# Kernel optimization log

Measured on AMD Instinct MI355X. Metric: run time of the kernel, lower is better.

The kernel has to match this reference:

```python
import jax, jax.numpy as jnp
import numpy as np

N_NODES = 50000
N_EDGES = 640000
F = 128          # feat_dims == hidden_dims == out_channels
L = 5            # num_layers of GatedGraphConv


def setup_inputs() -> dict:
    key = jax.random.key(0)
    ks = jax.random.split(key, 9)
    s = 1.0 / np.sqrt(F)
    x = jax.random.normal(ks[0], (N_NODES, F), dtype=jnp.float32)
    edge_index = jax.random.randint(ks[1], (2, N_EDGES), 0, N_NODES, dtype=jnp.int64)
    weight = jax.random.uniform(ks[2], (L, F, F), jnp.float32, -s, s)   # per-layer linear
    w_ih = jax.random.uniform(ks[3], (3 * F, F), jnp.float32, -s, s)     # GRUCell input weights
    w_hh = jax.random.uniform(ks[4], (3 * F, F), jnp.float32, -s, s)     # GRUCell hidden weights
    b_ih = jax.random.uniform(ks[5], (3 * F,), jnp.float32, -s, s)
    b_hh = jax.random.uniform(ks[6], (3 * F,), jnp.float32, -s, s)
    lin_w = jax.random.uniform(ks[7], (1, F), jnp.float32, -s, s)
    lin_b = jax.random.uniform(ks[8], (1,), jnp.float32, -s, s)
    return {"x": x, "edge_index": edge_index, "weight": weight,
            "w_ih": w_ih, "w_hh": w_hh, "b_ih": b_ih, "b_hh": b_hh,
            "lin_w": lin_w, "lin_b": lin_b}


def _gru_cell(m, h, w_ih, w_hh, b_ih, b_hh):
    gi = m @ w_ih.T + b_ih          # [N, 3F]
    gh = h @ w_hh.T + b_hh          # [N, 3F]
    i_r, i_z, i_n = jnp.split(gi, 3, axis=-1)
    h_r, h_z, h_n = jnp.split(gh, 3, axis=-1)
    r = jax.nn.sigmoid(i_r + h_r)
    z = jax.nn.sigmoid(i_z + h_z)
    n = jnp.tanh(i_n + r * h_n)
    return (1.0 - z) * n + z * h


def reference(x, edge_index, weight, w_ih, w_hh, b_ih, b_hh, lin_w, lin_b):
    src = edge_index[0]   # message source (x_j)
    dst = edge_index[1]   # aggregation target
    n_nodes = x.shape[0]
    h = x  # in_channels == out_channels, no padding needed
    for i in range(L):
        m = h @ weight[i]                                   # [N, F]
        agg = jax.ops.segment_sum(m[src], dst, num_segments=n_nodes)  # add-aggregate
        h = _gru_cell(agg, h, w_ih, w_hh, b_ih, b_hh)
    out = jax.nn.relu(h) @ lin_w.T + lin_b                  # [N, 1]
    return out
```

## Files before the change

### kernel.cpp

```cpp
#include <hip/hip_runtime.h>

typedef float f32x4 __attribute__((ext_vector_type(4)));
typedef __bf16 bf16x8 __attribute__((ext_vector_type(8)));
typedef unsigned short u16x8 __attribute__((ext_vector_type(8)));

#define F 128

__device__ __forceinline__ unsigned short bf16_rne(float f) {
  unsigned u = __float_as_uint(f);
  u += 0x7FFFu + ((u >> 16) & 1u);
  return (unsigned short)(u >> 16);
}
__device__ __forceinline__ float bf16f(unsigned short s) {
  return __uint_as_float((unsigned)s << 16);
}

__global__ void split8_kernel(const float* __restrict__ in,
                              unsigned short* __restrict__ hi, unsigned short* __restrict__ lo,
                              int n8) {
  int i = blockIdx.x * 256 + threadIdx.x;
  if (i >= n8) return;
  const float4* p = (const float4*)in + 2 * (size_t)i;
  float4 a = p[0], b = p[1];
  float v[8] = {a.x, a.y, a.z, a.w, b.x, b.y, b.z, b.w};
  u16x8 vh, vl;
#pragma unroll
  for (int e = 0; e < 8; ++e) {
    unsigned short x = bf16_rne(v[e]);
    vh[e] = x;
    vl[e] = bf16_rne(v[e] - bf16f(x));
  }
  *(u16x8*)(hi + 8 * (size_t)i) = vh;
  *(u16x8*)(lo + 8 * (size_t)i) = vl;
}

__device__ __forceinline__ int pidx(int j, int k) {
  int ks = k >> 5;
  int lane = (j & 15) | (((k >> 3) & 3) << 4);
  return (ks * 24 + (j >> 4)) * 512 + lane * 8 + (k & 7);
}

__global__ void prep_w_kernel(const float* __restrict__ W, const float* __restrict__ w_ih,
                              const float* __restrict__ w_hh,
                              unsigned short* __restrict__ WcT_hi, unsigned short* __restrict__ WcT_lo,
                              unsigned short* __restrict__ Whh_hi, unsigned short* __restrict__ Whh_lo,
                              int L) {
  int idx = blockIdx.x * 256 + threadIdx.x;
  const int per_layer = 384 * 128;
  if (idx < L * per_layer) {
    int t = idx / per_layer;
    int r = idx - t * per_layer;
    int j = r >> 7;
    int k = r & 127;
    const float* wi = w_ih + (size_t)j * 128;
    const float* wk = W + (size_t)t * 16384 + (size_t)k * 128;
    float acc = 0.f;
#pragma unroll 4
    for (int c = 0; c < 128; ++c) acc = fmaf(wk[c], wi[c], acc);
    unsigned short x = bf16_rne(acc);
    int p = t * per_layer + pidx(j, k);
    WcT_hi[p] = x;
    WcT_lo[p] = bf16_rne(acc - bf16f(x));
  } else if (idx < L * per_layer + per_layer) {
    int r = idx - L * per_layer;
    int j = r >> 7, k = r & 127;
    float v = w_hh[r];
    unsigned short x = bf16_rne(v);
    int p = pidx(j, k);
    Whh_hi[p] = x;
    Whh_lo[p] = bf16_rne(v - bf16f(x));
  }
}

__global__ void hist_kernel(const int* __restrict__ ei, int* __restrict__ cnt, int E) {
  int e = blockIdx.x * 256 + threadIdx.x;
  if (e < E) atomicAdd(&cnt[ei[E + e]], 1);
}

__global__ void scan1_kernel(const int* __restrict__ cnt, int* __restrict__ exscan,
                             int* __restrict__ chunk_sums, int N) {
  __shared__ int tmp[256];
  int i = blockIdx.x * 256 + threadIdx.x;
  int v = (i < N) ? cnt[i] : 0;
  tmp[threadIdx.x] = v;
  __syncthreads();
#pragma unroll
  for (int off = 1; off < 256; off <<= 1) {
    int a = (threadIdx.x >= off) ? tmp[threadIdx.x - off] : 0;
    __syncthreads();
    tmp[threadIdx.x] += a;
    __syncthreads();
  }
  if (i < N) exscan[i] = tmp[threadIdx.x] - v;
  if (threadIdx.x == 255) chunk_sums[blockIdx.x] = tmp[255];
}

__global__ void scan2_kernel(int* __restrict__ chunk_sums, int nchunk) {
  __shared__ int tmp[256];
  int v = (threadIdx.x < nchunk) ? chunk_sums[threadIdx.x] : 0;
  tmp[threadIdx.x] = v;
  __syncthreads();
#pragma unroll
  for (int off = 1; off < 256; off <<= 1) {
    int a = (threadIdx.x >= off) ? tmp[threadIdx.x - off] : 0;
    __syncthreads();
    tmp[threadIdx.x] += a;
    __syncthreads();
  }
  if (threadIdx.x < nchunk) chunk_sums[threadIdx.x] = tmp[threadIdx.x] - v;
}

__global__ void finalize_rowptr_kernel(const int* __restrict__ exscan,
                                       const int* __restrict__ chunk_sums,
                                       int* __restrict__ rowptr, int* __restrict__ cursor,
                                       int N, int E) {
  int i = blockIdx.x * 256 + threadIdx.x;
  if (i < N) {
    int v = exscan[i] + chunk_sums[i >> 8];
    rowptr[i] = v;
    cursor[i] = v;
  }
  if (i == N) rowptr[N] = E;
}

__global__ void place_kernel(const int* __restrict__ ei, int* __restrict__ cursor,
                             int* __restrict__ csr_src, int E) {
  int e = blockIdx.x * 256 + threadIdx.x;
  if (e >= E) return;
  int pos = atomicAdd(&cursor[ei[E + e]], 1);
  csr_src[pos] = ei[e];
}

__global__ __launch_bounds__(256) void gather_kernel(
    const unsigned* __restrict__ hh, const unsigned* __restrict__ hl,
    const int* __restrict__ rowptr, const int* __restrict__ csr_src,
    unsigned* __restrict__ shi, unsigned* __restrict__ slo, int N) {
  int node = blockIdx.x * 4 + (threadIdx.x >> 6);
  if (node >= N) return;
  int d = threadIdx.x & 63;
  int beg = rowptr[node], end = rowptr[node + 1];
  float a0 = 0.f, a1 = 0.f;
  int j = beg;
  for (; j + 4 <= end; j += 4) {
    int s0 = csr_src[j], s1 = csr_src[j + 1], s2 = csr_src[j + 2], s3 = csr_src[j + 3];
    unsigned h0 = hh[(size_t)s0 * 64 + d], l0 = hl[(size_t)s0 * 64 + d];
    unsigned h1 = hh[(size_t)s1 * 64 + d], l1 = hl[(size_t)s1 * 64 + d];
    unsigned h2 = hh[(size_t)s2 * 64 + d], l2 = hl[(size_t)s2 * 64 + d];
    unsigned h3 = hh[(size_t)s3 * 64 + d], l3 = hl[(size_t)s3 * 64 + d];
    a0 += bf16f(h0 & 0xffff) + bf16f(l0 & 0xffff);
    a1 += bf16f(h0 >> 16) + bf16f(l0 >> 16);
    a0 += bf16f(h1 & 0xffff) + bf16f(l1 & 0xffff);
    a1 += bf16f(h1 >> 16) + bf16f(l1 >> 16);
    a0 += bf16f(h2 & 0xffff) + bf16f(l2 & 0xffff);
    a1 += bf16f(h2 >> 16) + bf16f(l2 >> 16);
    a0 += bf16f(h3 & 0xffff) + bf16f(l3 & 0xffff);
    a1 += bf16f(h3 >> 16) + bf16f(l3 >> 16);
  }
  for (; j < end; ++j) {
    int s0 = csr_src[j];
    unsigned h0 = hh[(size_t)s0 * 64 + d], l0 = hl[(size_t)s0 * 64 + d];
    a0 += bf16f(h0 & 0xffff) + bf16f(l0 & 0xffff);
    a1 += bf16f(h0 >> 16) + bf16f(l0 >> 16);
  }
  unsigned short x0 = bf16_rne(a0), x1 = bf16_rne(a1);
  unsigned short y0 = bf16_rne(a0 - bf16f(x0)), y1 = bf16_rne(a1 - bf16f(x1));
  size_t o = (size_t)node * 64 + d;
  shi[o] = (unsigned)x0 | ((unsigned)x1 << 16);
  slo[o] = (unsigned)y0 | ((unsigned)y1 << 16);
}

__global__ __launch_bounds__(512, 2) void gemm_gru_kernel(
    const unsigned short* __restrict__ s_hi, const unsigned short* __restrict__ s_lo,
    const unsigned short* __restrict__ h_hi, const unsigned short* __restrict__ h_lo,
    const unsigned short* __restrict__ Bc_hi, const unsigned short* __restrict__ Bc_lo,
    const unsigned short* __restrict__ Bh_hi, const unsigned short* __restrict__ Bh_lo,
    const float* __restrict__ bih, const float* __restrict__ bhh,
    unsigned short* __restrict__ h_hi_out, unsigned short* __restrict__ h_lo_out, int N) {
  const int w    = threadIdx.x >> 6;
  const int lane = threadIdx.x & 63;
  const int rh   = w >> 2;
  const int g0   = (w & 3) * 32;
  const int lrow = lane & 15;
  const int row0 = blockIdx.x * 64 + rh * 32;
  const int lane8 = lane * 8;

  size_t a_base[2];
#pragma unroll
  for (int t = 0; t < 2; ++t) {
    int ar = row0 + t * 16 + lrow;
    if (ar >= N) ar = N - 1;
    a_base[t] = (size_t)ar * F + (lane >> 4) * 8;
  }

  f32x4 acc[24];
#pragma unroll
  for (int i = 0; i < 24; ++i) acc[i] = (f32x4){0.f, 0.f, 0.f, 0.f};

#pragma unroll
  for (int ks = 0; ks < 4; ++ks) {
    bf16x8 bch[6], bcl[6], bhh_[6], bhl[6];
#pragma unroll
    for (int g = 0; g < 6; ++g) {
      const int cb = g0 + (g / 3) * 16 + (g % 3) * 128;
      const size_t pf = ((size_t)(ks * 24 + (cb >> 4)) * 512) + lane8;
      bch[g]  = *(const bf16x8*)(Bc_hi + pf);
      bcl[g]  = *(const bf16x8*)(Bc_lo + pf);
      bhh_[g] = *(const bf16x8*)(Bh_hi + pf);
      bhl[g]  = *(const bf16x8*)(Bh_lo + pf);
    }
    bf16x8 ash[2], asl[2], ahh[2], ahl[2];
#pragma unroll
    for (int t = 0; t < 2; ++t) {
      const size_t ao = a_base[t] + ks * 32;
      ash[t] = *(const bf16x8*)(s_hi + ao);
      asl[t] = *(const bf16x8*)(s_lo + ao);
      ahh[t] = *(const bf16x8*)(h_hi + ao);
      ahl[t] = *(const bf16x8*)(h_lo + ao);
    }
#pragma unroll
    for (int t = 0; t < 2; ++t) {
#pragma unroll
      for (int g = 0; g < 6; ++g) {
        const int ia = (t * 6 + g) * 2;
        acc[ia] = __builtin_amdgcn_mfma_f32_16x16x32_bf16(ash[t], bch[g], acc[ia], 0, 0, 0);
        acc[ia] = __builtin_amdgcn_mfma_f32_16x16x32_bf16(asl[t], bch[g], acc[ia], 0, 0, 0);
        acc[ia] = __builtin_amdgcn_mfma_f32_16x16x32_bf16(ash[t], bcl[g], acc[ia], 0, 0, 0);
        acc[ia + 1] = __builtin_amdgcn_mfma_f32_16x16x32_bf16(ahh[t], bhh_[g], acc[ia + 1], 0, 0, 0);
        acc[ia + 1] = __builtin_amdgcn_mfma_f32_16x16x32_bf16(ahl[t], bhh_[g], acc[ia + 1], 0, 0, 0);
        acc[ia + 1] = __builtin_amdgcn_mfma_f32_16x16x32_bf16(ahh[t], bhl[g], acc[ia + 1], 0, 0, 0);
      }
    }
  }

  __syncthreads();

#pragma unroll
  for (int t = 0; t < 2; ++t) {
    const int rbase = row0 + t * 16 + (lane >> 4) * 4;
#pragma unroll
    for (int t2 = 0; t2 < 2; ++t2) {
      const int c = g0 + t2 * 16 + lrow;
      const float br  = bih[c] + bhh[c];
      const float bz  = bih[128 + c] + bhh[128 + c];
      const float bni = bih[256 + c];
      const float bnh = bhh[256 + c];
#pragma unroll
      for (int i = 0; i < 4; ++i) {
        const int r = rbase + i;
        if (r < N) {
          const int b0 = (t * 6 + t2 * 3) * 2;
          const float c1r = acc[b0 + 0][i], c2r = acc[b0 + 1][i];
          const float c1z = acc[b0 + 2][i], c2z = acc[b0 + 3][i];
          const float c1n = acc[b0 + 4][i], c2n = acc[b0 + 5][i];
          const float rr = 1.f / (1.f + __expf(-(c1r + c2r + br)));
          const float zz = 1.f / (1.f + __expf(-(c1z + c2z + bz)));
          const float nn = tanhf(c1n + bni + rr * (c2n + bnh));
          const size_t o = (size_t)r * F + c;
          const float hold = bf16f(h_hi_out[o]) + bf16f(h_lo_out[o]);
          const float hn = (1.f - zz) * nn + zz * hold;
          const unsigned short x = bf16_rne(hn);
          h_hi_out[o] = x;
          h_lo_out[o] = bf16_rne(hn - bf16f(x));
        }
      }
    }
  }
}

__global__ void final_kernel(const unsigned* __restrict__ hh, const unsigned* __restrict__ hl,
                             const float* __restrict__ lin_w,
                             const float* __restrict__ lin_b, float* __restrict__ out, int N) {
  int n = blockIdx.x * 4 + (threadIdx.x >> 6);
  if (n >= N) return;
  int lane = threadIdx.x & 63;
  unsigned wh = hh[(size_t)n * 64 + lane], wl = hl[(size_t)n * 64 + lane];
  float v0 = bf16f(wh & 0xffff) + bf16f(wl & 0xffff);
  float v1 = bf16f(wh >> 16) + bf16f(wl >> 16);
  float2 wv = *(const float2*)(lin_w + lane * 2);
  float sum = fmaxf(v0, 0.f) * wv.x + fmaxf(v1, 0.f) * wv.y;
#pragma unroll
  for (int o = 32; o; o >>= 1) sum += __shfl_xor(sum, o, 64);
  if (lane == 0) out[n] = sum + lin_b[0];
}

extern "C" void kernel_launch(void* const* d_in, const int* in_sizes, int n_in,
                              void* d_out, int out_size, void* d_ws, size_t ws_size,
                              hipStream_t stream) {
  const float* x     = (const float*)d_in[0];
  const int*   ei    = (const int*)d_in[1];
  const float* W     = (const float*)d_in[2];
  const float* w_ih  = (const float*)d_in[3];
  const float* w_hh  = (const float*)d_in[4];
  const float* b_ih  = (const float*)d_in[5];
  const float* b_hh  = (const float*)d_in[6];
  const float* lin_w = (const float*)d_in[7];
  const float* lin_b = (const float*)d_in[8];

  const int N = in_sizes[0] / F;
  const int E = in_sizes[1] / 2;
  const int L = in_sizes[2] / (F * F);
  const size_t NF = (size_t)N * F;
  const int PW = 384 * 128;

  char* p = (char*)d_ws;
  unsigned short* h_hi = (unsigned short*)p; p += NF * 2;
  unsigned short* h_lo = (unsigned short*)p; p += NF * 2;
  unsigned short* s_hi = (unsigned short*)p; p += NF * 2;
  unsigned short* s_lo = (unsigned short*)p; p += NF * 2;
  unsigned short* WcT_hi = (unsigned short*)p; p += (size_t)L * PW * 2;
  unsigned short* WcT_lo = (unsigned short*)p; p += (size_t)L * PW * 2;
  unsigned short* Whh_hi = (unsigned short*)p; p += PW * 2;
  unsigned short* Whh_lo = (unsigned short*)p; p += PW * 2;
  int* cnt       = (int*)p; p += (size_t)N * 4;
  int* exscan    = (int*)p; p += (size_t)N * 4;
  int* chunk     = (int*)p; p += 256 * 4;
  int* rowptr    = (int*)p; p += ((size_t)N + 1) * 4;
  int* cursor    = (int*)p; p += (size_t)N * 4;
  int* csr_src   = (int*)p; p += (size_t)E * 4;

  const int n8 = (int)(NF / 8);
  const int split_blocks = (n8 + 255) / 256;
  const int prep_blocks = (L * PW + PW + 255) / 256;
  const int edge_blocks = (E + 255) / 256;
  const int nchunk = (N + 255) / 256;
  const int gemm_blocks = (N + 63) / 64;
  const int node4_blocks = (N + 3) / 4;

  split8_kernel<<<split_blocks, 256, 0, stream>>>(x, h_hi, h_lo, n8);
  prep_w_kernel<<<prep_blocks, 256, 0, stream>>>(W, w_ih, w_hh, WcT_hi, WcT_lo,
                                                 Whh_hi, Whh_lo, L);

  hipMemsetAsync(cnt, 0, (size_t)N * 4, stream);
  hist_kernel<<<edge_blocks, 256, 0, stream>>>(ei, cnt, E);
  scan1_kernel<<<nchunk, 256, 0, stream>>>(cnt, exscan, chunk, N);
  scan2_kernel<<<1, 256, 0, stream>>>(chunk, nchunk);
  finalize_rowptr_kernel<<<(N + 256) / 256, 256, 0, stream>>>(exscan, chunk, rowptr, cursor, N, E);
  place_kernel<<<edge_blocks, 256, 0, stream>>>(ei, cursor, csr_src, E);

  for (int t = 0; t < L; ++t) {
    gather_kernel<<<node4_blocks, 256, 0, stream>>>(
        (const unsigned*)h_hi, (const unsigned*)h_lo, rowptr, csr_src,
        (unsigned*)s_hi, (unsigned*)s_lo, N);
    gemm_gru_kernel<<<gemm_blocks, 512, 0, stream>>>(
        s_hi, s_lo, h_hi, h_lo,
        WcT_hi + (size_t)t * PW, WcT_lo + (size_t)t * PW, Whh_hi, Whh_lo,
        b_ih, b_hh, h_hi, h_lo, N);
  }

  final_kernel<<<node4_blocks, 256, 0, stream>>>(
      (const unsigned*)h_hi, (const unsigned*)h_lo, lin_w, lin_b, (float*)d_out, N);
}
```

Baseline: 772.7 us.

## Stage GEMM operands through LDS with async double-buffered loads and K-major layout

```diff
diff --git a/kernel.cpp b/kernel.cpp
--- a/kernel.cpp
+++ b/kernel.cpp
@@ -15,12 +15,14 @@
   return __uint_as_float((unsigned)s << 16);
 }
 
+
 __global__ void split8_kernel(const float* __restrict__ in,
                               unsigned short* __restrict__ hi, unsigned short* __restrict__ lo,
-                              int n8) {
+                              int N) {
   int i = blockIdx.x * 256 + threadIdx.x;
-  if (i >= n8) return;
-  const float4* p = (const float4*)in + 2 * (size_t)i;
+  if (i >= N * 16) return;
+  int node = i >> 4, f8 = i & 15;
+  const float4* p = (const float4*)(in + (size_t)node * F + f8 * 8);
   float4 a = p[0], b = p[1];
   float v[8] = {a.x, a.y, a.z, a.w, b.x, b.y, b.z, b.w};
   u16x8 vh, vl;
@@ -30,46 +32,39 @@
     vh[e] = x;
     vl[e] = bf16_rne(v[e] - bf16f(x));
   }
-  *(u16x8*)(hi + 8 * (size_t)i) = vh;
-  *(u16x8*)(lo + 8 * (size_t)i) = vl;
-}
-
-__device__ __forceinline__ int pidx(int j, int k) {
-  int ks = k >> 5;
-  int lane = (j & 15) | (((k >> 3) & 3) << 4);
-  return (ks * 24 + (j >> 4)) * 512 + lane * 8 + (k & 7);
+  size_t o = ((size_t)(f8 >> 2) * N + node) * 32 + (f8 & 3) * 8;
+  *(u16x8*)(hi + o) = vh;
+  *(u16x8*)(lo + o) = vl;
 }
 
 __global__ void prep_w_kernel(const float* __restrict__ W, const float* __restrict__ w_ih,
                               const float* __restrict__ w_hh,
-                              unsigned short* __restrict__ WcT_hi, unsigned short* __restrict__ WcT_lo,
-                              unsigned short* __restrict__ Whh_hi, unsigned short* __restrict__ Whh_lo,
-                              int L) {
+                              unsigned short* __restrict__ Bpack, int L) {
   int idx = blockIdx.x * 256 + threadIdx.x;
-  const int per_layer = 384 * 128;
-  if (idx < L * per_layer) {
-    int t = idx / per_layer;
-    int r = idx - t * per_layer;
-    int j = r >> 7;
-    int k = r & 127;
+  if (idx >= L * 8 * 12 * 2 * 512) return;
+  int low = idx & 511;
+  int e = low & 7, lane = low >> 3;
+  int rest = idx >> 9;
+  int ap = rest & 1; rest >>= 1;
+  int ct = rest % 12; rest /= 12;
+  int ph = rest & 7, t = rest >> 3;
+  int j = (ph & 1) * 192 + ct * 16 + (lane & 15);
+  int k = (ph >> 1) * 32 + (lane >> 4) * 8 + e;
+  float v;
+  if (ap == 0) {
     const float* wi = w_ih + (size_t)j * 128;
     const float* wk = W + (size_t)t * 16384 + (size_t)k * 128;
     float acc = 0.f;
 #pragma unroll 4
     for (int c = 0; c < 128; ++c) acc = fmaf(wk[c], wi[c], acc);
-    unsigned short x = bf16_rne(acc);
-    int p = t * per_layer + pidx(j, k);
-    WcT_hi[p] = x;
-    WcT_lo[p] = bf16_rne(acc - bf16f(x));
-  } else if (idx < L * per_layer + per_layer) {
-    int r = idx - L * per_layer;
-    int j = r >> 7, k = r & 127;
-    float v = w_hh[r];
-    unsigned short x = bf16_rne(v);
-    int p = pidx(j, k);
-    Whh_hi[p] = x;
-    Whh_lo[p] = bf16_rne(v - bf16f(x));
-  }
+    v = acc;
+  } else {
+    v = w_hh[(size_t)j * 128 + k];
+  }
+  unsigned short x = bf16_rne(v);
+  size_t base = (size_t)t * 196608 + (size_t)((ph * 12 + ct) * 4 + ap * 2) * 512 + lane * 8 + e;
+  Bpack[base] = x;
+  Bpack[base + 512] = bf16_rne(v - bf16f(x));
 }
 
 __global__ void hist_kernel(const int* __restrict__ ei, int* __restrict__ cnt, int E) {
@@ -138,124 +133,251 @@
   int node = blockIdx.x * 4 + (threadIdx.x >> 6);
   if (node >= N) return;
   int d = threadIdx.x & 63;
-  int beg = rowptr[node], end = rowptr[node + 1];
+  const size_t pb = (size_t)(d >> 4) * N * 16 + (d & 15);
+  int j = rowptr[node], end = rowptr[node + 1];
   float a0 = 0.f, a1 = 0.f;
-  int j = beg;
+  for (; j + 8 <= end; j += 8) {
+#pragma unroll
+    for (int u = 0; u < 8; ++u) {
+      int s = csr_src[j + u];
+      unsigned hv = hh[pb + (size_t)s * 16];
+      unsigned lv = hl[pb + (size_t)s * 16];
+      a0 += bf16f((unsigned short)(hv & 0xffff)) + bf16f((unsigned short)(lv & 0xffff));
+      a1 += bf16f((unsigned short)(hv >> 16)) + bf16f((unsigned short)(lv >> 16));
+    }
+  }
   for (; j + 4 <= end; j += 4) {
-    int s0 = csr_src[j], s1 = csr_src[j + 1], s2 = csr_src[j + 2], s3 = csr_src[j + 3];
-    unsigned h0 = hh[(size_t)s0 * 64 + d], l0 = hl[(size_t)s0 * 64 + d];
-    unsigned h1 = hh[(size_t)s1 * 64 + d], l1 = hl[(size_t)s1 * 64 + d];
-    unsigned h2 = hh[(size_t)s2 * 64 + d], l2 = hl[(size_t)s2 * 64 + d];
-    unsigned h3 = hh[(size_t)s3 * 64 + d], l3 = hl[(size_t)s3 * 64 + d];
-    a0 += bf16f(h0 & 0xffff) + bf16f(l0 & 0xffff);
-    a1 += bf16f(h0 >> 16) + bf16f(l0 >> 16);
-    a0 += bf16f(h1 & 0xffff) + bf16f(l1 & 0xffff);
-    a1 += bf16f(h1 >> 16) + bf16f(l1 >> 16);
-    a0 += bf16f(h2 & 0xffff) + bf16f(l2 & 0xffff);
-    a1 += bf16f(h2 >> 16) + bf16f(l2 >> 16);
-    a0 += bf16f(h3 & 0xffff) + bf16f(l3 & 0xffff);
-    a1 += bf16f(h3 >> 16) + bf16f(l3 >> 16);
+#pragma unroll
+    for (int u = 0; u < 4; ++u) {
+      int s = csr_src[j + u];
+      unsigned hv = hh[pb + (size_t)s * 16];
+      unsigned lv = hl[pb + (size_t)s * 16];
+      a0 += bf16f((unsigned short)(hv & 0xffff)) + bf16f((unsigned short)(lv & 0xffff));
+      a1 += bf16f((unsigned short)(hv >> 16)) + bf16f((unsigned short)(lv >> 16));
+    }
   }
   for (; j < end; ++j) {
-    int s0 = csr_src[j];
-    unsigned h0 = hh[(size_t)s0 * 64 + d], l0 = hl[(size_t)s0 * 64 + d];
-    a0 += bf16f(h0 & 0xffff) + bf16f(l0 & 0xffff);
-    a1 += bf16f(h0 >> 16) + bf16f(l0 >> 16);
+    int s = csr_src[j];
+    unsigned hv = hh[pb + (size_t)s * 16];
+    unsigned lv = hl[pb + (size_t)s * 16];
+    a0 += bf16f((unsigned short)(hv & 0xffff)) + bf16f((unsigned short)(lv & 0xffff));
+    a1 += bf16f((unsigned short)(hv >> 16)) + bf16f((unsigned short)(lv >> 16));
   }
   unsigned short x0 = bf16_rne(a0), x1 = bf16_rne(a1);
   unsigned short y0 = bf16_rne(a0 - bf16f(x0)), y1 = bf16_rne(a1 - bf16f(x1));
-  size_t o = (size_t)node * 64 + d;
-  shi[o] = (unsigned)x0 | ((unsigned)x1 << 16);
-  slo[o] = (unsigned)y0 | ((unsigned)y1 << 16);
-}
-
-__global__ __launch_bounds__(512, 2) void gemm_gru_kernel(
-    const unsigned short* __restrict__ s_hi, const unsigned short* __restrict__ s_lo,
-    const unsigned short* __restrict__ h_hi, const unsigned short* __restrict__ h_lo,
-    const unsigned short* __restrict__ Bc_hi, const unsigned short* __restrict__ Bc_lo,
-    const unsigned short* __restrict__ Bh_hi, const unsigned short* __restrict__ Bh_lo,
+  shi[pb + (size_t)node * 16] = (unsigned)x0 | ((unsigned)x1 << 16);
+  slo[pb + (size_t)node * 16] = (unsigned)y0 | ((unsigned)y1 << 16);
+}
+
+#define BBUF(b) ((b) * 49152)
+#define ABUF 98304
+
+__device__ __forceinline__ void g2l(const void* g, void* l) {
+  __builtin_amdgcn_global_load_lds((const __attribute__((address_space(1))) void*)g,
+                                   (__attribute__((address_space(3))) void*)l, 16, 0, 0);
+}
+
+#define DS_READ_A()                                                                  \
+  {                                                                                  \
+    _Pragma("unroll") for (int t = 0; t < 2; ++t) {                                  \
+      int row = rh * 32 + t * 16 + lrow;                                             \
+      const unsigned char* ab = lds + ABUF + row * 64 + ((kq ^ (row & 3)) << 4);     \
+      ash[t] = *(const bf16x8*)(ab);                                                 \
+      asl[t] = *(const bf16x8*)(ab + 4096);                                          \
+      ahh[t] = *(const bf16x8*)(ab + 8192);                                          \
+      ahl[t] = *(const bf16x8*)(ab + 12288);                                         \
+    }                                                                                \
+  }
+
+#define DS_READ_B(bb)                                                                \
+  bf16x8 bch[3], bcl[3], bh2[3], bhl[3];                                             \
+  {                                                                                  \
+    _Pragma("unroll") for (int jj = 0; jj < 3; ++jj) {                               \
+      const unsigned char* bp = lds + BBUF(bb) + (q + jj * 4) * 4096 + lane * 16;    \
+      bch[jj] = *(const bf16x8*)(bp);                                                \
+      bcl[jj] = *(const bf16x8*)(bp + 1024);                                         \
+      bh2[jj] = *(const bf16x8*)(bp + 2048);                                         \
+      bhl[jj] = *(const bf16x8*)(bp + 3072);                                         \
+    }                                                                                \
+  }
+
+#define MFMA_BLOCK(half)                                                             \
+  {                                                                                  \
+    const int PT[2][3] = {{0, 0, 1}, {1, 2, 2}};                                     \
+    const int FG[2][3] = {{0, 1, 0}, {1, 0, 1}};                                     \
+    _Pragma("unroll") for (int jj = 0; jj < 3; ++jj) {                               \
+      const int part = PT[half][jj], fgi = FG[half][jj];                             \
+      _Pragma("unroll") for (int t = 0; t < 2; ++t) {                                \
+        const int ai = ((t * 2 + fgi) * 3 + part) * 2;                               \
+        acc[ai] = __builtin_amdgcn_mfma_f32_16x16x32_bf16(ash[t], bch[jj], acc[ai], 0, 0, 0); \
+        acc[ai] = __builtin_amdgcn_mfma_f32_16x16x32_bf16(asl[t], bch[jj], acc[ai], 0, 0, 0); \
+        acc[ai] = __builtin_amdgcn_mfma_f32_16x16x32_bf16(ash[t], bcl[jj], acc[ai], 0, 0, 0); \
+        acc[ai + 1] = __builtin_amdgcn_mfma_f32_16x16x32_bf16(ahh[t], bh2[jj], acc[ai + 1], 0, 0, 0); \
+        acc[ai + 1] = __builtin_amdgcn_mfma_f32_16x16x32_bf16(ahl[t], bh2[jj], acc[ai + 1], 0, 0, 0); \
+        acc[ai + 1] = __builtin_amdgcn_mfma_f32_16x16x32_bf16(ahh[t], bhl[jj], acc[ai + 1], 0, 0, 0); \
+      }                                                                              \
+    }                                                                                \
+  }
+
+#define WAIT_LGKM()                                                                  \
+  asm volatile("s_waitcnt lgkmcnt(0)" ::: "memory");                                 \
+  __builtin_amdgcn_sched_barrier(0);
+
+__global__ __launch_bounds__(512, 1) void gemm_gru_kernel(
+    const unsigned short* s_hi, const unsigned short* s_lo,
+    const unsigned short* h_hi, const unsigned short* h_lo,
+    const unsigned short* __restrict__ Bpack,
     const float* __restrict__ bih, const float* __restrict__ bhh,
-    unsigned short* __restrict__ h_hi_out, unsigned short* __restrict__ h_lo_out, int N) {
-  const int w    = threadIdx.x >> 6;
-  const int lane = threadIdx.x & 63;
-  const int rh   = w >> 2;
-  const int g0   = (w & 3) * 32;
-  const int lrow = lane & 15;
-  const int row0 = blockIdx.x * 64 + rh * 32;
-  const int lane8 = lane * 8;
-
-  size_t a_base[2];
+    unsigned short* h_hi_out, unsigned short* h_lo_out, int N) {
+  __shared__ __align__(1024) unsigned char lds[114688];
+  const int tid = threadIdx.x, w = tid >> 6, lane = tid & 63;
+  const int q = w & 3, rh = w >> 2, lrow = lane & 15, kq = lane >> 4;
+  const int row0 = blockIdx.x * 64;
+
+  auto stageB = [&](int ph, int b) {
+    const unsigned char* g = (const unsigned char*)Bpack + (size_t)ph * 49152 + w * 6144 + lane * 16;
+    unsigned char* l = lds + BBUF(b) + w * 6144;
+#pragma unroll
+    for (int i = 0; i < 6; ++i) g2l(g + i * 1024, l + i * 1024);
+  };
+  auto stageA = [&](int ks) {
+    const int arr = w >> 1;
+    const unsigned short* ap = (arr == 0) ? s_hi : (arr == 1) ? s_lo : (arr == 2) ? h_hi : h_lo;
+    const int slot = (lane & 3) ^ ((lane >> 2) & 3);
+    unsigned char* l = lds + ABUF + arr * 4096;
+#pragma unroll
+    for (int i = 0; i < 2; ++i) {
+      const int chunk = (w & 1) * 2 + i;
+      int gr = row0 + chunk * 16 + (lane >> 2);
+      if (gr >= N) gr = N - 1;
+      const unsigned char* g = (const unsigned char*)ap + ((size_t)ks * N + gr) * 64 + slot * 16;
+      g2l(g, l + chunk * 1024);
+    }
+  };
+
+  f32x4 acc[24];
+#pragma unroll
+  for (int i = 0; i < 24; ++i) acc[i] = (f32x4){0.f, 0.f, 0.f, 0.f};
+  bf16x8 ash[2], asl[2], ahh[2], ahl[2];
+
+  stageB(0, 0);
+  stageA(0);
+  stageB(1, 1);
+  asm volatile("s_waitcnt vmcnt(6)" ::: "memory");
+  __builtin_amdgcn_s_barrier();
+
+  {
+    DS_READ_A();
+    DS_READ_B(0);
+    WAIT_LGKM();
+    __builtin_amdgcn_s_barrier();
+    stageB(2, 0);
+    stageA(1);
+    __builtin_amdgcn_s_setprio(1);
+    MFMA_BLOCK(0);
+    __builtin_amdgcn_s_setprio(0);
+    asm volatile("s_waitcnt vmcnt(8)" ::: "memory");
+    __builtin_amdgcn_s_barrier();
+  }
+  {
+    DS_READ_B(1);
+    WAIT_LGKM();
+    __builtin_amdgcn_s_barrier();
+    stageB(3, 1);
+    __builtin_amdgcn_s_setprio(1);
+    MFMA_BLOCK(1);
+    __builtin_amdgcn_s_setprio(0);
+    asm volatile("s_waitcnt vmcnt(6)" ::: "memory");
+    __builtin_amdgcn_s_barrier();
+  }
+  {
+    DS_READ_A();
+    DS_READ_B(0);
+    WAIT_LGKM();
+    __builtin_amdgcn_s_barrier();
+    stageB(4, 0);
+    stageA(2);
+    __builtin_amdgcn_s_setprio(1);
+    MFMA_BLOCK(0);
+    __builtin_amdgcn_s_setprio(0);
+    asm volatile("s_waitcnt vmcnt(8)" ::: "memory");
+    __builtin_amdgcn_s_barrier();
+  }
+  {
+    DS_READ_B(1);
+    WAIT_LGKM();
+    __builtin_amdgcn_s_barrier();
+    stageB(5, 1);
+    __builtin_amdgcn_s_setprio(1);
+    MFMA_BLOCK(1);
+    __builtin_amdgcn_s_setprio(0);
+    asm volatile("s_waitcnt vmcnt(6)" ::: "memory");
+    __builtin_amdgcn_s_barrier();
+  }
+  {
+    DS_READ_A();
+    DS_READ_B(0);
+    WAIT_LGKM();
+    __builtin_amdgcn_s_barrier();
+    stageB(6, 0);
+    stageA(3);
+    __builtin_amdgcn_s_setprio(1);
+    MFMA_BLOCK(0);
+    __builtin_amdgcn_s_setprio(0);
+    asm volatile("s_waitcnt vmcnt(8)" ::: "memory");
+    __builtin_amdgcn_s_barrier();
+  }
+  {
+    DS_READ_B(1);
+    WAIT_LGKM();
+    __builtin_amdgcn_s_barrier();
+    stageB(7, 1);
+    __builtin_amdgcn_s_setprio(1);
+    MFMA_BLOCK(1);
+    __builtin_amdgcn_s_setprio(0);
+    asm volatile("s_waitcnt vmcnt(6)" ::: "memory");
+    __builtin_amdgcn_s_barrier();
+  }
+  {
+    DS_READ_A();
+    DS_READ_B(0);
+    WAIT_LGKM();
+    __builtin_amdgcn_s_barrier();
+    __builtin_amdgcn_s_setprio(1);
+    MFMA_BLOCK(0);
+    __builtin_amdgcn_s_setprio(0);
+    asm volatile("s_waitcnt vmcnt(0)" ::: "memory");
+    __builtin_amdgcn_s_barrier();
+  }
+  {
+    DS_READ_B(1);
+    __builtin_amdgcn_s_setprio(1);
+    MFMA_BLOCK(1);
+    __builtin_amdgcn_s_setprio(0);
+  }
+
 #pragma unroll
   for (int t = 0; t < 2; ++t) {
-    int ar = row0 + t * 16 + lrow;
-    if (ar >= N) ar = N - 1;
-    a_base[t] = (size_t)ar * F + (lane >> 4) * 8;
-  }
-
-  f32x4 acc[24];
-#pragma unroll
-  for (int i = 0; i < 24; ++i) acc[i] = (f32x4){0.f, 0.f, 0.f, 0.f};
-
-#pragma unroll
-  for (int ks = 0; ks < 4; ++ks) {
-    bf16x8 bch[6], bcl[6], bhh_[6], bhl[6];
-#pragma unroll
-    for (int g = 0; g < 6; ++g) {
-      const int cb = g0 + (g / 3) * 16 + (g % 3) * 128;
-      const size_t pf = ((size_t)(ks * 24 + (cb >> 4)) * 512) + lane8;
-      bch[g]  = *(const bf16x8*)(Bc_hi + pf);
-      bcl[g]  = *(const bf16x8*)(Bc_lo + pf);
-      bhh_[g] = *(const bf16x8*)(Bh_hi + pf);
-      bhl[g]  = *(const bf16x8*)(Bh_lo + pf);
-    }
-    bf16x8 ash[2], asl[2], ahh[2], ahl[2];
-#pragma unroll
-    for (int t = 0; t < 2; ++t) {
-      const size_t ao = a_base[t] + ks * 32;
-      ash[t] = *(const bf16x8*)(s_hi + ao);
-      asl[t] = *(const bf16x8*)(s_lo + ao);
-      ahh[t] = *(const bf16x8*)(h_hi + ao);
-      ahl[t] = *(const bf16x8*)(h_lo + ao);
-    }
-#pragma unroll
-    for (int t = 0; t < 2; ++t) {
-#pragma unroll
-      for (int g = 0; g < 6; ++g) {
-        const int ia = (t * 6 + g) * 2;
-        acc[ia] = __builtin_amdgcn_mfma_f32_16x16x32_bf16(ash[t], bch[g], acc[ia], 0, 0, 0);
-        acc[ia] = __builtin_amdgcn_mfma_f32_16x16x32_bf16(asl[t], bch[g], acc[ia], 0, 0, 0);
-        acc[ia] = __builtin_amdgcn_mfma_f32_16x16x32_bf16(ash[t], bcl[g], acc[ia], 0, 0, 0);
-        acc[ia + 1] = __builtin_amdgcn_mfma_f32_16x16x32_bf16(ahh[t], bhh_[g], acc[ia + 1], 0, 0, 0);
-        acc[ia + 1] = __builtin_amdgcn_mfma_f32_16x16x32_bf16(ahl[t], bhh_[g], acc[ia + 1], 0, 0, 0);
-        acc[ia + 1] = __builtin_amdgcn_mfma_f32_16x16x32_bf16(ahh[t], bhl[g], acc[ia + 1], 0, 0, 0);
-      }
-    }
-  }
-
-  __syncthreads();
-
-#pragma unroll
-  for (int t = 0; t < 2; ++t) {
-    const int rbase = row0 + t * 16 + (lane >> 4) * 4;
-#pragma unroll
-    for (int t2 = 0; t2 < 2; ++t2) {
-      const int c = g0 + t2 * 16 + lrow;
-      const float br  = bih[c] + bhh[c];
-      const float bz  = bih[128 + c] + bhh[128 + c];
-      const float bni = bih[256 + c];
-      const float bnh = bhh[256 + c];
+    const int rb = row0 + rh * 32 + t * 16 + kq * 4;
+#pragma unroll
+    for (int fi = 0; fi < 2; ++fi) {
+      const int fg = q + fi * 4;
+      const int c = fg * 16 + lrow;
+      const float br = bih[c] + bhh[c];
+      const float bz = bih[128 + c] + bhh[128 + c];
+      const float bni = bih[256 + c], bnh = bhh[256 + c];
 #pragma unroll
       for (int i = 0; i < 4; ++i) {
-        const int r = rbase + i;
+        const int r = rb + i;
         if (r < N) {
-          const int b0 = (t * 6 + t2 * 3) * 2;
-          const float c1r = acc[b0 + 0][i], c2r = acc[b0 + 1][i];
-          const float c1z = acc[b0 + 2][i], c2z = acc[b0 + 3][i];
-          const float c1n = acc[b0 + 4][i], c2n = acc[b0 + 5][i];
+          const int a0 = ((t * 2 + fi) * 3) * 2;
+          const float c1r = acc[a0 + 0][i], c2r = acc[a0 + 1][i];
+          const float c1z = acc[a0 + 2][i], c2z = acc[a0 + 3][i];
+          const float c1n = acc[a0 + 4][i], c2n = acc[a0 + 5][i];
           const float rr = 1.f / (1.f + __expf(-(c1r + c2r + br)));
           const float zz = 1.f / (1.f + __expf(-(c1z + c2z + bz)));
           const float nn = tanhf(c1n + bni + rr * (c2n + bnh));
-          const size_t o = (size_t)r * F + c;
+          const size_t o = ((size_t)(fg >> 1) * N + r) * 32 + (fg & 1) * 16 + lrow;
           const float hold = bf16f(h_hi_out[o]) + bf16f(h_lo_out[o]);
           const float hn = (1.f - zz) * nn + zz * hold;
           const unsigned short x = bf16_rne(hn);
@@ -272,15 +394,16 @@
                              const float* __restrict__ lin_b, float* __restrict__ out, int N) {
   int n = blockIdx.x * 4 + (threadIdx.x >> 6);
   if (n >= N) return;
-  int lane = threadIdx.x & 63;
-  unsigned wh = hh[(size_t)n * 64 + lane], wl = hl[(size_t)n * 64 + lane];
-  float v0 = bf16f(wh & 0xffff) + bf16f(wl & 0xffff);
-  float v1 = bf16f(wh >> 16) + bf16f(wl >> 16);
-  float2 wv = *(const float2*)(lin_w + lane * 2);
-  float sum = fmaxf(v0, 0.f) * wv.x + fmaxf(v1, 0.f) * wv.y;
-#pragma unroll
-  for (int o = 32; o; o >>= 1) sum += __shfl_xor(sum, o, 64);
-  if (lane == 0) out[n] = sum + lin_b[0];
+  int d = threadIdx.x & 63;
+  size_t o = ((size_t)(d >> 4) * N + n) * 16 + (d & 15);
+  unsigned wh = hh[o], wl = hl[o];
+  float v0 = bf16f((unsigned short)(wh & 0xffff)) + bf16f((unsigned short)(wl & 0xffff));
+  float v1 = bf16f((unsigned short)(wh >> 16)) + bf16f((unsigned short)(wl >> 16));
+  int f0 = (d >> 4) * 32 + 2 * (d & 15);
+  float sum = fmaxf(v0, 0.f) * lin_w[f0] + fmaxf(v1, 0.f) * lin_w[f0 + 1];
+#pragma unroll
+  for (int s = 32; s; s >>= 1) sum += __shfl_xor(sum, s, 64);
+  if (d == 0) out[n] = sum + lin_b[0];
 }
 
 extern "C" void kernel_launch(void* const* d_in, const int* in_sizes, int n_in,
@@ -300,35 +423,29 @@
   const int E = in_sizes[1] / 2;
   const int L = in_sizes[2] / (F * F);
   const size_t NF = (size_t)N * F;
-  const int PW = 384 * 128;
 
   char* p = (char*)d_ws;
   unsigned short* h_hi = (unsigned short*)p; p += NF * 2;
   unsigned short* h_lo = (unsigned short*)p; p += NF * 2;
   unsigned short* s_hi = (unsigned short*)p; p += NF * 2;
   unsigned short* s_lo = (unsigned short*)p; p += NF * 2;
-  unsigned short* WcT_hi = (unsigned short*)p; p += (size_t)L * PW * 2;
-  unsigned short* WcT_lo = (unsigned short*)p; p += (size_t)L * PW * 2;
-  unsigned short* Whh_hi = (unsigned short*)p; p += PW * 2;
-  unsigned short* Whh_lo = (unsigned short*)p; p += PW * 2;
-  int* cnt       = (int*)p; p += (size_t)N * 4;
-  int* exscan    = (int*)p; p += (size_t)N * 4;
-  int* chunk     = (int*)p; p += 256 * 4;
-  int* rowptr    = (int*)p; p += ((size_t)N + 1) * 4;
-  int* cursor    = (int*)p; p += (size_t)N * 4;
-  int* csr_src   = (int*)p; p += (size_t)E * 4;
-
-  const int n8 = (int)(NF / 8);
-  const int split_blocks = (n8 + 255) / 256;
-  const int prep_blocks = (L * PW + PW + 255) / 256;
+  unsigned short* Bpack = (unsigned short*)p; p += (size_t)L * 196608 * 2;
+  int* cnt     = (int*)p; p += (size_t)N * 4;
+  int* exscan  = (int*)p; p += (size_t)N * 4;
+  int* chunk   = (int*)p; p += 256 * 4;
+  int* rowptr  = (int*)p; p += ((size_t)N + 1) * 4;
+  int* cursor  = (int*)p; p += (size_t)N * 4;
+  int* csr_src = (int*)p; p += (size_t)E * 4;
+
+  const int split_blocks = (N * 16 + 255) / 256;
+  const int prep_blocks = (L * 8 * 12 * 2 * 512 + 255) / 256;
   const int edge_blocks = (E + 255) / 256;
   const int nchunk = (N + 255) / 256;
   const int gemm_blocks = (N + 63) / 64;
   const int node4_blocks = (N + 3) / 4;
 
-  split8_kernel<<<split_blocks, 256, 0, stream>>>(x, h_hi, h_lo, n8);
-  prep_w_kernel<<<prep_blocks, 256, 0, stream>>>(W, w_ih, w_hh, WcT_hi, WcT_lo,
-                                                 Whh_hi, Whh_lo, L);
+  split8_kernel<<<split_blocks, 256, 0, stream>>>(x, h_hi, h_lo, N);
+  prep_w_kernel<<<prep_blocks, 256, 0, stream>>>(W, w_ih, w_hh, Bpack, L);
 
   hipMemsetAsync(cnt, 0, (size_t)N * 4, stream);
   hist_kernel<<<edge_blocks, 256, 0, stream>>>(ei, cnt, E);
@@ -342,8 +459,7 @@
         (const unsigned*)h_hi, (const unsigned*)h_lo, rowptr, csr_src,
         (unsigned*)s_hi, (unsigned*)s_lo, N);
     gemm_gru_kernel<<<gemm_blocks, 512, 0, stream>>>(
-        s_hi, s_lo, h_hi, h_lo,
-        WcT_hi + (size_t)t * PW, WcT_lo + (size_t)t * PW, Whh_hi, Whh_lo,
+        s_hi, s_lo, h_hi, h_lo, Bpack + (size_t)t * 196608,
         b_ih, b_hh, h_hi, h_lo, N);
   }
 
```

Measured after the change: 979.5 us. +26.8%, slower.
